# Kernel optimization log

Hardware: AMD Instinct MI355X
Metric: run time of the kernel (lower is better)

The kernel has to match this reference:

```python
import jax, jax.numpy as jnp
import numpy as np
from jax import lax

B, C_IN, C, H, W = 4, 256, 128, 64, 64
UP = (128, 128)
EPS = 1e-8  # torch CosineSimilarity eps


def _conv(x, w, b, p):
    y = lax.conv_general_dilated(x, w, (1, 1), [(p, p), (p, p)],
                                 dimension_numbers=('NCHW', 'OIHW', 'NCHW'))
    return y + b[None, :, None, None]


def _stdconv(x, w, b, s, o, p=0):
    # StdConv.forward = bn(act(conv(x))); eval-mode BatchNorm folded to per-channel affine (s, o)
    y = jax.nn.relu(_conv(x, w, b, p))
    return y * s[None, :, None, None] + o[None, :, None, None]


def _forward(t1, t2, t1_w, t1_b, t2_w, t2_b,
             df_res_w, df_res_b, df_res_s, df_res_o,
             df_b0_w, df_b0_b, df_b0_s, df_b0_o,
             df_b1_w, df_b1_b, df_b1_s, df_b1_o,
             df_fu_w, df_fu_b, df_fu_s, df_fu_o,
             br1_w, br1_b, br2_w, br2_b,
             fu_w, fu_b, fu_s, fu_o):
    Bs, _, Hs, Ws = t1.shape
    res1 = _conv(t1, t1_w, t1_b, 0)                      # [B,C,H,W]
    res2 = _conv(t2, t2_w, t2_b, 0)
    # torch .contiguous().view(B,-1,c) on NCHW: plain row-major reshape (NOT a transpose)
    f1 = res1.reshape(Bs, Hs * Ws, C)
    f2 = res2.reshape(Bs, Hs * Ws, C)
    num = jnp.sum(f1 * f2, axis=-1)
    den = jnp.maximum(jnp.linalg.norm(f1, axis=-1) * jnp.linalg.norm(f2, axis=-1), EPS)
    sim = (num / den)[..., None]                          # [B,HW,1]
    dif_w = 1.0 - sim

    def to_img(f):  # permute(0,2,1).view(B,C,H,W)
        return jnp.transpose(f, (0, 2, 1)).reshape(Bs, C, Hs, Ws)

    sim1 = to_img(f1 * sim) + res1
    sim2 = to_img(f2 * sim) + res2
    dif1 = to_img(f1 * dif_w) + res1
    dif2 = to_img(f2 * dif_w) + res2
    # AvgPool2d(kernel=2, stride=2)
    simp = jnp.abs(sim1 - sim2).reshape(Bs, C, Hs // 2, 2, Ws // 2, 2).mean(axis=(3, 5))
    # InceptionConv(2C -> C, branch=2)
    x = jnp.concatenate([dif1, dif2], axis=1)
    r = _stdconv(x, df_res_w, df_res_b, df_res_s, df_res_o, 0)
    b0 = _stdconv(r, df_b0_w, df_b0_b, df_b0_s, df_b0_o, 1)   # 3x3
    b1 = _stdconv(r, df_b1_w, df_b1_b, df_b1_s, df_b1_o, 2)   # 5x5
    dif = _stdconv(jnp.concatenate([b0, b1], axis=1), df_fu_w, df_fu_b, df_fu_s, df_fu_o, 0) + r
    N = (Hs // 2) * (Ws // 2)
    attn = simp.reshape(Bs, N, C)                         # [B,N,C]

    def branch_attn(inc):
        br = inc.reshape(Bs, C, Hs * Ws)                  # [B,C,HW]
        a = jax.nn.softmax(jnp.einsum('bnc,bcm->bnm', attn, br), axis=-1)  # [B,N,HW]
        return jnp.einsum('bnc,bnm->bcm', attn, a).reshape(Bs, C, Hs, Ws) + inc

    inc1 = _conv(dif, br1_w, br1_b, 1)
    inc2 = _conv(dif, br2_w, br2_b, 2)
    a1 = branch_attn(inc1)
    a2 = branch_attn(inc2)
    fused = _stdconv(jnp.concatenate([a1, a2], axis=1), fu_w, fu_b, fu_s, fu_o, 0) + dif
    # F.interpolate(..., mode='bilinear', align_corners=False) == jax bilinear resize
    return jax.image.resize(fused, (Bs, C, UP[0], UP[1]), method='bilinear')


def setup_inputs():
    key = jax.random.key(0)
    ks = iter(jax.random.split(key, 40))
    rn = lambda shape, sc=0.05: jax.random.normal(next(ks), shape, jnp.float32) * sc
    return {
        't1': jax.random.normal(next(ks), (B, C_IN, H, W), jnp.float32),
        't2': jax.random.normal(next(ks), (B, C_IN, H, W), jnp.float32),
        't1_w': rn((C, C_IN, 1, 1)), 't1_b': rn((C,)),
        't2_w': rn((C, C_IN, 1, 1)), 't2_b': rn((C,)),
        'df_res_w': rn((C, 2 * C, 1, 1)), 'df_res_b': rn((C,)), 'df_res_s': 1.0 + rn((C,)), 'df_res_o': rn((C,)),
        'df_b0_w': rn((C // 2, C, 3, 3)), 'df_b0_b': rn((C // 2,)), 'df_b0_s': 1.0 + rn((C // 2,)), 'df_b0_o': rn((C // 2,)),
        'df_b1_w': rn((C // 2, C, 5, 5)), 'df_b1_b': rn((C // 2,)), 'df_b1_s': 1.0 + rn((C // 2,)), 'df_b1_o': rn((C // 2,)),
        'df_fu_w': rn((C, C, 1, 1)), 'df_fu_b': rn((C,)), 'df_fu_s': 1.0 + rn((C,)), 'df_fu_o': rn((C,)),
        'br1_w': rn((C, C, 3, 3)), 'br1_b': rn((C,)),
        'br2_w': rn((C, C, 5, 5)), 'br2_b': rn((C,)),
        'fu_w': rn((C, 2 * C, 1, 1)), 'fu_b': rn((C,)), 'fu_s': 1.0 + rn((C,)), 'fu_o': rn((C,)),
    }


def reference(t1, t2, t1_w, t1_b, t2_w, t2_b,
              df_res_w, df_res_b, df_res_s, df_res_o,
              df_b0_w, df_b0_b, df_b0_s, df_b0_o,
              df_b1_w, df_b1_b, df_b1_s, df_b1_o,
              df_fu_w, df_fu_b, df_fu_s, df_fu_o,
              br1_w, br1_b, br2_w, br2_b,
              fu_w, fu_b, fu_s, fu_o):
    return _forward(t1, t2, t1_w, t1_b, t2_w, t2_b,
                    df_res_w, df_res_b, df_res_s, df_res_o,
                    df_b0_w, df_b0_b, df_b0_s, df_b0_o,
                    df_b1_w, df_b1_b, df_b1_s, df_b1_o,
                    df_fu_w, df_fu_b, df_fu_s, df_fu_o,
                    br1_w, br1_b, br2_w, br2_b,
                    fu_w, fu_b, fu_s, fu_o)
```

## Files before the change

### kernel.cpp

```cpp
#include <hip/hip_runtime.h>
#include <math.h>

#define HW 4096

typedef __attribute__((ext_vector_type(8))) short short8;
typedef __attribute__((ext_vector_type(4))) float floatx4;
typedef __attribute__((ext_vector_type(2))) float floatx2;

__device__ inline unsigned short f2bf(float f) {
    unsigned int u = __float_as_uint(f);
    unsigned int r = (u + 0x7fffu + ((u >> 16) & 1u)) >> 16;
    return (unsigned short)r;
}
__device__ inline float bf2f(unsigned short u) {
    return __uint_as_float(((unsigned int)u) << 16);
}


__device__ inline void prepack_dev(const float* __restrict__ w, unsigned short* __restrict__ wp,
                                   int CO, int CI, int KK, int i)
{
    if (i >= CO * CI * KK) return;
    int ci = i % CI;
    int t = i / CI;
    int co = t % CO;
    int kk = t / CO;
    int ti = (kk * (CO >> 4) + (co >> 4)) * (CI >> 5) + (ci >> 5);
    wp[(size_t)ti * 512 + ((ci >> 3) & 3) * 128 + (co & 15) * 8 + (ci & 7)]
        = f2bf(w[(co * CI + ci) * KK + kk]);
}

__global__ void setup_kernel(uint4* __restrict__ zp, int zn,
                             const float* __restrict__ w0, unsigned short* __restrict__ wp0,
                             const float* __restrict__ w1, unsigned short* __restrict__ wp1,
                             const float* __restrict__ w2, unsigned short* __restrict__ wp2,
                             const float* __restrict__ w3, unsigned short* __restrict__ wp3)
{
    int bx = blockIdx.x, tid = threadIdx.x;
    if (bx < 2312) {
        int i = bx * 256 + tid;
        if (i < zn) zp[i] = make_uint4(0u, 0u, 0u, 0u);
    } else if (bx < 2600) {
        prepack_dev(w0, wp0, 64, 128, 9,  (bx - 2312) * 256 + tid);
    } else if (bx < 3400) {
        prepack_dev(w1, wp1, 64, 128, 25, (bx - 2600) * 256 + tid);
    } else if (bx < 3976) {
        prepack_dev(w2, wp2, 128, 128, 9, (bx - 3400) * 256 + tid);
    } else {
        prepack_dev(w3, wp3, 128, 128, 25,(bx - 3976) * 256 + tid);
    }
}

__global__ void __launch_bounds__(256)
conv1x1_v2(const float* __restrict__ in, const float* __restrict__ w,
           const float* __restrict__ bias, float* __restrict__ out,
           int CI, int CO, int do_affine,
           const float* __restrict__ s, const float* __restrict__ o,
           const float* __restrict__ addbuf, unsigned short* __restrict__ xt)
{
    __shared__ float wl[2048];
    int tid = threadIdx.x;
    int c0 = blockIdx.y * 8;
    int b = blockIdx.z;
    for (int i = tid; i < CI * 8; i += 256) {
        int k = i & 7, ci = i >> 3;
        wl[i] = w[(c0 + k) * CI + ci];
    }
    __syncthreads();
    int m = blockIdx.x * 512 + tid * 2;
    floatx2 acc[8];
#pragma unroll
    for (int k = 0; k < 8; ++k) {
        float bv = bias[c0 + k];
        acc[k] = (floatx2){bv, bv};
    }
    const float* inb = in + (size_t)b * CI * HW + m;
#pragma unroll 4
    for (int ci = 0; ci < CI; ++ci) {
        floatx2 v = *(const floatx2*)(inb + (size_t)ci * HW);
#pragma unroll
        for (int k = 0; k < 8; ++k) acc[k] += wl[ci * 8 + k] * v;
    }
#pragma unroll
    for (int k = 0; k < 8; ++k) {
        floatx2 v = acc[k];
        if (do_affine) {
            float sc = s[c0 + k], of = o[c0 + k];
            v[0] = fmaxf(v[0], 0.f) * sc + of;
            v[1] = fmaxf(v[1], 0.f) * sc + of;
        }
        size_t oidx = ((size_t)(b * CO + c0 + k)) * HW + m;
        if (addbuf) v += *(const floatx2*)(addbuf + oidx);
        *(floatx2*)(out + oidx) = v;
        acc[k] = v;
    }
    if (xt) {
#pragma unroll
        for (int r = 0; r < 2; ++r) {
            int mm = m + r;
            union { unsigned short u16[8]; uint4 q; } pk;
#pragma unroll
            for (int k = 0; k < 8; ++k) pk.u16[k] = f2bf(acc[k][r]);
            int h = mm >> 6, wc = mm & 63;
            *(uint4*)(xt + ((size_t)(b * 16 + (c0 >> 3)) * 4624 + (h + 2) * 68 + (wc + 2)) * 8) = pk.q;
        }
    }
}

template<int K, int CO, int NB, int MS>
__global__ void __launch_bounds__(256)
convk_mfma(const unsigned short* __restrict__ xt, const unsigned short* __restrict__ wp,
           const float* __restrict__ bias, float* __restrict__ out,
           int OB, int co_off, int do_affine,
           const float* __restrict__ s, const float* __restrict__ o,
           unsigned short* __restrict__ incT)
{
    constexpr int CI = 128;
    constexpr int PAD = K / 2;
    constexpr int RO = 2 - PAD;
    constexpr int MT = 4 / MS;
    constexpr int CO16 = CO >> 4;
    constexpr int CI32 = CI >> 5;
    int tid = threadIdx.x;
    int wave = tid >> 6, lane = tid & 63;
    int h = blockIdx.x / MS, msb = blockIdx.x % MS;
    int b = blockIdx.y;
    int co0 = wave * 16 * NB;
    int n = lane & 15, q = lane >> 4;
    floatx4 acc[MT][NB];
#pragma unroll
    for (int mt = 0; mt < MT; ++mt)
#pragma unroll
        for (int nt = 0; nt < NB; ++nt) acc[mt][nt] = (floatx4){0.f, 0.f, 0.f, 0.f};

    const unsigned short* xb = xt + (size_t)(b * 16) * 4624 * 8;
    int mbase = msb * MT * 16;
    for (int ci0 = 0; ci0 < CI; ci0 += 32) {
#pragma unroll
        for (int kh = 0; kh < K; ++kh) {
            const unsigned short* xrow = xb + (size_t)(((ci0 >> 3) + q) * 4624 + (h + kh + RO) * 68 + RO) * 8;
            const unsigned short* wkh = wp + ((size_t)(kh * K) * CO16 * CI32 + (ci0 >> 5)) * 512 + lane * 8;
#pragma unroll
            for (int kw = 0; kw < K; ++kw) {
                short8 bfr[NB];
#pragma unroll
                for (int nt = 0; nt < NB; ++nt)
                    bfr[nt] = *(const short8*)(wkh + (size_t)((kw * CO16 + (co0 >> 4) + nt) * CI32) * 512);
#pragma unroll
                for (int mt = 0; mt < MT; ++mt) {
                    short8 afr = *(const short8*)(xrow + (mbase + mt * 16 + n + kw) * 8);
#pragma unroll
                    for (int nt = 0; nt < NB; ++nt)
                        acc[mt][nt] = __builtin_amdgcn_mfma_f32_16x16x32_bf16(afr, bfr[nt], acc[mt][nt], 0, 0, 0);
                }
            }
        }
    }
    int px0 = h * 64 + mbase + q * 4;
#pragma unroll
    for (int nt = 0; nt < NB; ++nt) {
        int co = co0 + nt * 16 + n;
        float bi = bias[co];
        float sc = do_affine ? s[co] : 1.f;
        float of = do_affine ? o[co] : 0.f;
        float* ob = out + ((size_t)(b * OB + co_off + co)) * HW;
        unsigned short* tb = incT ? incT + (size_t)b * 524288 : nullptr;
        int cpart = (co >> 5) * 512 + ((co >> 3) & 3) * 128 + (co & 7);
#pragma unroll
        for (int mt = 0; mt < MT; ++mt)
#pragma unroll
            for (int r = 0; r < 4; ++r) {
                int px = px0 + mt * 16 + r;
                float v = acc[mt][nt][r] + bi;
                if (do_affine) v = fmaxf(v, 0.f) * sc + of;
                ob[px] = v;
                if (incT) tb[(size_t)((px >> 4) * 2048 + cpart + (px & 15) * 8)] = f2bf(v);
            }
    }
}

__global__ void sim_kernel(const float* __restrict__ r1, const float* __restrict__ r2,
                           float* __restrict__ sim)
{
    int gw = blockIdx.x * 4 + (threadIdx.x >> 6);
    int lane = threadIdx.x & 63;
    int b = gw >> 12, n = gw & 4095;
    const float* p1 = r1 + (size_t)b * 524288 + (size_t)n * 128;
    const float* p2 = r2 + (size_t)b * 524288 + (size_t)n * 128;
    float a0 = p1[lane], a1 = p1[lane + 64];
    float b0 = p2[lane], b1 = p2[lane + 64];
    float dot = a0 * b0 + a1 * b1;
    float n1 = a0 * a0 + a1 * a1;
    float n2 = b0 * b0 + b1 * b1;
    for (int m = 32; m; m >>= 1) {
        dot += __shfl_xor(dot, m);
        n1  += __shfl_xor(n1, m);
        n2  += __shfl_xor(n2, m);
    }
    if (lane == 0) sim[b * 4096 + n] = dot / fmaxf(sqrtf(n1) * sqrtf(n2), 1e-8f);
}

__global__ void __launch_bounds__(256)
x_kernel2(const float* __restrict__ r1, const float* __restrict__ r2,
          const float* __restrict__ sim, float* __restrict__ xo)
{
    __shared__ float ls1[32 * 129], ls2[32 * 129];
    int b = blockIdx.y, p0 = blockIdx.x * 32, tid = threadIdx.x;
    const float* F1 = r1 + (size_t)b * 524288;
    const float* F2 = r2 + (size_t)b * 524288;
    for (int i = tid; i < 32 * 128; i += 256) {
        int p = i >> 7, c = i & 127;
        ls1[p * 129 + c] = F1[p0 * 128 + i];
        ls2[p * 129 + c] = F2[p0 * 128 + i];
    }
    __syncthreads();
    for (int j = tid; j < 256 * 32; j += 256) {
        int p = j & 31, cc = j >> 5;
        int c = cc & 127;
        float sv = sim[b * 4096 + p0 + p];
        const float* F = (cc & 128) ? F2 : F1;
        float t1v = ((cc & 128) ? ls2 : ls1)[p * 129 + c];
        xo[(size_t)b * 1048576 + (size_t)cc * 4096 + p0 + p] = t1v * (1.f - sv) + F[(size_t)c * 4096 + p0 + p];
    }
}

__global__ void __launch_bounds__(256)
simp_kernel3(const float* __restrict__ r1, const float* __restrict__ r2,
             const float* __restrict__ sim, unsigned short* __restrict__ attn_pk)
{
    __shared__ float lsd[64 * 33];
    int b = blockIdx.y, h2 = blockIdx.x, cg = blockIdx.z, tid = threadIdx.x;
    const float* F1 = r1 + (size_t)b * 524288;
    const float* F2 = r2 + (size_t)b * 524288;
    const float* sb = sim + b * 4096;
    int w2 = tid & 31, cl = tid >> 5;
    float acc[4] = {};
    for (int dh = 0; dh < 2; ++dh) {
        int prow = h2 * 128 + dh * 64;
        __syncthreads();
        for (int i = tid; i < 64 * 32; i += 256) {
            int p = i >> 5, c = i & 31;
            size_t gi = (size_t)(prow + p) * 128 + cg * 32 + c;
            lsd[p * 33 + c] = F1[gi] - F2[gi];
        }
        __syncthreads();
#pragma unroll
        for (int k = 0; k < 4; ++k) {
            int c = cl + 8 * k;
            int cG = cg * 32 + c;
#pragma unroll
            for (int dw = 0; dw < 2; ++dw) {
                int pl = 2 * w2 + dw;
                int p = prow + pl;
                float d = lsd[pl * 33 + c] * sb[p]
                        + (F1[(size_t)cG * 4096 + p] - F2[(size_t)cG * 4096 + p]);
                acc[k] += fabsf(d);
            }
        }
    }
#pragma unroll
    for (int k = 0; k < 4; ++k) {
        int cG = cg * 32 + cl + 8 * k;
        int f = cG * 1024 + h2 * 32 + w2;
        int n = f >> 7, c = f & 127;
        attn_pk[(size_t)b * 131072 + ((n >> 4) * 4 + (c >> 5)) * 512
                + ((c >> 3) & 3) * 128 + (n & 15) * 8 + (c & 7)] = f2bf(acc[k] * 0.25f);
    }
}

__global__ void __launch_bounds__(256)
attnA_pass1(const unsigned short* __restrict__ attn_pk,
            const unsigned short* __restrict__ incT1, const unsigned short* __restrict__ incT2,
            float* __restrict__ pmax, float* __restrict__ psum)
{
    __shared__ float lm[4][32], ls[4][32];
    int pair = blockIdx.y;
    int b = pair & 3, br = pair >> 2;
    int z = blockIdx.z;
    int tid = threadIdx.x;
    int wave = tid >> 6, lane = tid & 63;
    int n0 = blockIdx.x * 32;
    int q = lane >> 4;
    int col = lane & 15;
    const unsigned short* apk = attn_pk + (size_t)b * 131072 + (size_t)blockIdx.x * 4096 + lane * 8;
    short8 afrA[4], afrB[4];
#pragma unroll
    for (int kc = 0; kc < 4; ++kc) {
        afrA[kc] = *(const short8*)(apk + kc * 512);
        afrB[kc] = *(const short8*)(apk + 2048 + kc * 512);
    }
    const unsigned short* ibp = (br ? incT2 : incT1) + (size_t)b * 524288 + lane * 8;
    short8 bbuf[2][4];
    {
        const unsigned short* brow = ibp + (size_t)(z * 64 + wave * 16) * 2048;
#pragma unroll
        for (int kc = 0; kc < 4; ++kc) bbuf[0][kc] = *(const short8*)(brow + kc * 512);
        brow += 2048;
#pragma unroll
        for (int kc = 0; kc < 4; ++kc) bbuf[1][kc] = *(const short8*)(brow + kc * 512);
    }
    float rmA[4], rsA[4], rmB[4], rsB[4];
#pragma unroll
    for (int r = 0; r < 4; ++r) { rmA[r] = -3.0e38f; rsA[r] = 0.f; rmB[r] = -3.0e38f; rsB[r] = 0.f; }
#pragma unroll
    for (int mt = 0; mt < 16; ++mt) {
        const int cur = mt & 1;
        floatx4 accA = (floatx4){0.f, 0.f, 0.f, 0.f};
        floatx4 accB = (floatx4){0.f, 0.f, 0.f, 0.f};
#pragma unroll
        for (int kc = 0; kc < 4; ++kc) {
            accA = __builtin_amdgcn_mfma_f32_16x16x32_bf16(afrA[kc], bbuf[cur][kc], accA, 0, 0, 0);
            accB = __builtin_amdgcn_mfma_f32_16x16x32_bf16(afrB[kc], bbuf[cur][kc], accB, 0, 0, 0);
        }
        if (mt < 14) {
            const unsigned short* brow = ibp + (size_t)(z * 64 + wave * 16 + mt + 2) * 2048;
#pragma unroll
            for (int kc = 0; kc < 4; ++kc) bbuf[cur][kc] = *(const short8*)(brow + kc * 512);
        }
#pragma unroll
        for (int r = 0; r < 4; ++r) {
            float vA = accA[r];
            float nmA = fmaxf(rmA[r], vA);
            rsA[r] = rsA[r] * __expf(rmA[r] - nmA) + __expf(vA - nmA);
            rmA[r] = nmA;
            float vB = accB[r];
            float nmB = fmaxf(rmB[r], vB);
            rsB[r] = rsB[r] * __expf(rmB[r] - nmB) + __expf(vB - nmB);
            rmB[r] = nmB;
        }
    }
#pragma unroll
    for (int d = 1; d < 16; d <<= 1) {
#pragma unroll
        for (int r = 0; r < 4; ++r) {
            float om = __shfl_xor(rmA[r], d);
            float os = __shfl_xor(rsA[r], d);
            float nm = fmaxf(rmA[r], om);
            rsA[r] = rsA[r] * __expf(rmA[r] - nm) + os * __expf(om - nm);
            rmA[r] = nm;
            om = __shfl_xor(rmB[r], d);
            os = __shfl_xor(rsB[r], d);
            nm = fmaxf(rmB[r], om);
            rsB[r] = rsB[r] * __expf(rmB[r] - nm) + os * __expf(om - nm);
            rmB[r] = nm;
        }
    }
    if (col == 0) {
#pragma unroll
        for (int r = 0; r < 4; ++r) {
            lm[wave][q * 4 + r] = rmA[r];      ls[wave][q * 4 + r] = rsA[r];
            lm[wave][16 + q * 4 + r] = rmB[r]; ls[wave][16 + q * 4 + r] = rsB[r];
        }
    }
    __syncthreads();
    if (tid < 32) {
        float bm = lm[0][tid], bs = ls[0][tid];
        for (int w = 1; w < 4; ++w) {
            float om = lm[w][tid], os = ls[w][tid];
            float nm = fmaxf(bm, om);
            bs = bs * __expf(bm - nm) + os * __expf(om - nm);
            bm = nm;
        }
        pmax[((size_t)pair * 4 + z) * 1024 + n0 + tid] = bm;
        psum[((size_t)pair * 4 + z) * 1024 + n0 + tid] = bs;
    }
}

__global__ void attnA_scale2(const unsigned short* __restrict__ attn_pk,
                             const float* __restrict__ pmax, const float* __restrict__ psum,
                             float* __restrict__ mx, unsigned short* __restrict__ attnS_pk)
{
    int i = blockIdx.x * 256 + threadIdx.x;
    int pair = i >> 17;
    int o = i & 131071;
    int j = o & 7, lane = (o >> 3) & 63, ct = (o >> 9) & 7, kcn = o >> 12;
    int c = ct * 16 + (lane & 15);
    int n = kcn * 32 + (lane >> 4) * 8 + j;
    int b = pair & 3;
    float bm = pmax[((size_t)pair * 4) * 1024 + n];
    float bs = psum[((size_t)pair * 4) * 1024 + n];
#pragma unroll
    for (int z = 1; z < 4; ++z) {
        float om = pmax[((size_t)pair * 4 + z) * 1024 + n];
        float os = psum[((size_t)pair * 4 + z) * 1024 + n];
        float nm = fmaxf(bm, om);
        bs = bs * __expf(bm - nm) + os * __expf(om - nm);
        bm = nm;
    }
    if (c == 0) mx[pair * 1024 + n] = bm;
    float rc = 1.f / bs;
    int ii = b * 131072 + ((n >> 4) * 4 + (c >> 5)) * 512
           + ((c >> 3) & 3) * 128 + (n & 15) * 8 + (c & 7);
    attnS_pk[(size_t)i] = f2bf(bf2f(attn_pk[ii]) * rc);
}

__global__ void __launch_bounds__(256)
attn_passB4(const unsigned short* __restrict__ attn_pk,
            const unsigned short* __restrict__ attnS_pk,
            const unsigned short* __restrict__ incT1, const unsigned short* __restrict__ incT2,
            const float* __restrict__ mx,
            const float* __restrict__ inc1, const float* __restrict__ inc2,
            float* __restrict__ abuf)
{
    __shared__ unsigned short lp[4][16 * 36];
    __shared__ float lred[2][2048];
    int pair = blockIdx.y;
    int b = pair & 3, br = pair >> 2;
    int tid = threadIdx.x;
    int wv = tid >> 6, lane = tid & 63;
    int q = lane >> 4, col = lane & 15;
    int msub = wv & 1, nh = wv >> 1;
    int m0 = blockIdx.x * 32 + msub * 16;
    int mtg = m0 >> 4;
    const unsigned short* ibp = (br ? incT2 : incT1) + (size_t)b * 524288 + lane * 8;
    short8 bfrS[4];
#pragma unroll
    for (int kc = 0; kc < 4; ++kc)
        bfrS[kc] = *(const short8*)(ibp + (size_t)(mtg * 4 + kc) * 512);
    const float* mxp = mx + pair * 1024 + nh * 512;
    const unsigned short* aspk = attnS_pk + (size_t)pair * 131072 + lane * 8;
    const unsigned short* apk = attn_pk + (size_t)b * 131072 + lane * 8;
    floatx4 oacc[8];
#pragma unroll
    for (int ct = 0; ct < 8; ++ct) oacc[ct] = (floatx4){0.f, 0.f, 0.f, 0.f};
    unsigned short* lw = lp[wv];

    short8 arP[2][2][4];
    short8 asP[2][8];
    floatx4 mxq[2][2];
    floatx4 sacc[2][2];

#pragma unroll
    for (int t = 0; t < 2; ++t)
#pragma unroll
        for (int kc = 0; kc < 4; ++kc)
            arP[0][t][kc] = *(const short8*)(apk + (size_t)(((nh * 32 + t) * 4 + kc)) * 512);
#pragma unroll
    for (int ct = 0; ct < 8; ++ct)
        asP[0][ct] = *(const short8*)(aspk + (size_t)((nh * 16) * 8 + ct) * 512);
#pragma unroll
    for (int t = 0; t < 2; ++t)
        mxq[0][t] = *(const floatx4*)(mxp + t * 16 + q * 4);
#pragma unroll
    for (int t = 0; t < 2; ++t) {
        floatx4 a = (floatx4){0.f, 0.f, 0.f, 0.f};
#pragma unroll
        for (int kc = 0; kc < 4; ++kc)
            a = __builtin_amdgcn_mfma_f32_16x16x32_bf16(arP[0][t][kc], bfrS[kc], a, 0, 0, 0);
        sacc[0][t] = a;
    }
#pragma unroll
    for (int t = 0; t < 2; ++t)
#pragma unroll
        for (int kc = 0; kc < 4; ++kc)
            arP[1][t][kc] = *(const short8*)(apk + (size_t)(((nh * 32 + 2 + t) * 4 + kc)) * 512);

#pragma unroll
    for (int nc = 0; nc < 16; ++nc) {
        const int cur = nc & 1, nxt = cur ^ 1;
#pragma unroll
        for (int t = 0; t < 2; ++t) {
            floatx4 sv = sacc[cur][t];
            floatx4 mv = mxq[cur][t];
            unsigned int p01 = (unsigned int)f2bf(__expf(sv[0] - mv[0]))
                             | ((unsigned int)f2bf(__expf(sv[1] - mv[1])) << 16);
            unsigned int p23 = (unsigned int)f2bf(__expf(sv[2] - mv[2]))
                             | ((unsigned int)f2bf(__expf(sv[3] - mv[3])) << 16);
            *(uint2*)&lw[col * 36 + t * 16 + q * 4] = make_uint2(p01, p23);
        }
        if (nc < 15) {
#pragma unroll
            for (int ct = 0; ct < 8; ++ct)
                asP[nxt][ct] = *(const short8*)(aspk + (size_t)(((nh * 16 + nc + 1) * 8 + ct)) * 512);
#pragma unroll
            for (int t = 0; t < 2; ++t)
                mxq[nxt][t] = *(const floatx4*)(mxp + (nc + 1) * 32 + t * 16 + q * 4);
        }
        short8 pb = *(const short8*)&lw[col * 36 + q * 8];
        if (nc < 15) {
#pragma unroll
            for (int t = 0; t < 2; ++t) {
                floatx4 a = (floatx4){0.f, 0.f, 0.f, 0.f};
#pragma unroll
                for (int kc = 0; kc < 4; ++kc)
                    a = __builtin_amdgcn_mfma_f32_16x16x32_bf16(arP[nxt][t][kc], bfrS[kc], a, 0, 0, 0);
                sacc[nxt][t] = a;
            }
        }
        if (nc < 14) {
#pragma unroll
            for (int t = 0; t < 2; ++t)
#pragma unroll
                for (int kc = 0; kc < 4; ++kc)
                    arP[cur][t][kc] = *(const short8*)(apk + (size_t)(((nh * 32 + (nc + 2) * 2 + t) * 4 + kc)) * 512);
        }
#pragma unroll
        for (int ct = 0; ct < 8; ++ct)
            oacc[ct] = __builtin_amdgcn_mfma_f32_16x16x32_bf16(asP[cur][ct], pb, oacc[ct], 0, 0, 0);
    }

    if (nh == 1) {
        float* lr = lred[msub];
#pragma unroll
        for (int ct = 0; ct < 8; ++ct)
#pragma unroll
            for (int r = 0; r < 4; ++r)
                lr[(ct * 16 + q * 4 + r) * 16 + col] = oacc[ct][r];
    }
    __syncthreads();
    if (nh == 0) {
        const float* lr = lred[msub];
        const float* resid = (br ? inc2 : inc1) + (size_t)b * 524288;
        float* op = abuf + ((size_t)(b * 256 + br * 128)) * 4096;
        int m = m0 + col;
#pragma unroll
        for (int ct = 0; ct < 8; ++ct)
#pragma unroll
            for (int r = 0; r < 4; ++r) {
                int row = ct * 16 + q * 4 + r;
                op[(size_t)row * 4096 + m] = oacc[ct][r] + lr[row * 16 + col]
                                           + resid[(size_t)row * 4096 + m];
            }
    }
}

__global__ void upsample_kernel(const float* __restrict__ in, float* __restrict__ out)
{
    int i = blockIdx.x * 256 + threadIdx.x;
    int x = i & 127, y = (i >> 7) & 127, bc = i >> 14;
    const float* ib = in + (size_t)bc * HW;
    float sy = 0.5f * y - 0.25f;
    float sx = 0.5f * x - 0.25f;
    int y0 = (int)floorf(sy); float ty = sy - y0;
    int x0 = (int)floorf(sx); float tx = sx - x0;
    int y0c = min(max(y0, 0), 63), y1c = min(max(y0 + 1, 0), 63);
    int x0c = min(max(x0, 0), 63), x1c = min(max(x0 + 1, 0), 63);
    float v00 = ib[y0c * 64 + x0c], v01 = ib[y0c * 64 + x1c];
    float v10 = ib[y1c * 64 + x0c], v11 = ib[y1c * 64 + x1c];
    out[i] = (1.f - ty) * ((1.f - tx) * v00 + tx * v01) + ty * ((1.f - tx) * v10 + tx * v11);
}

extern "C" void kernel_launch(void* const* d_in, const int* in_sizes, int n_in,
                              void* d_out, int out_size, void* d_ws, size_t ws_size,
                              hipStream_t stream)
{
    const float* t1       = (const float*)d_in[0];
    const float* t2       = (const float*)d_in[1];
    const float* t1_w     = (const float*)d_in[2];
    const float* t1_b     = (const float*)d_in[3];
    const float* t2_w     = (const float*)d_in[4];
    const float* t2_b     = (const float*)d_in[5];
    const float* df_res_w = (const float*)d_in[6];
    const float* df_res_b = (const float*)d_in[7];
    const float* df_res_s = (const float*)d_in[8];
    const float* df_res_o = (const float*)d_in[9];
    const float* df_b0_w  = (const float*)d_in[10];
    const float* df_b0_b  = (const float*)d_in[11];
    const float* df_b0_s  = (const float*)d_in[12];
    const float* df_b0_o  = (const float*)d_in[13];
    const float* df_b1_w  = (const float*)d_in[14];
    const float* df_b1_b  = (const float*)d_in[15];
    const float* df_b1_s  = (const float*)d_in[16];
    const float* df_b1_o  = (const float*)d_in[17];
    const float* df_fu_w  = (const float*)d_in[18];
    const float* df_fu_b  = (const float*)d_in[19];
    const float* df_fu_s  = (const float*)d_in[20];
    const float* df_fu_o  = (const float*)d_in[21];
    const float* br1_w    = (const float*)d_in[22];
    const float* br1_b    = (const float*)d_in[23];
    const float* br2_w    = (const float*)d_in[24];
    const float* br2_b    = (const float*)d_in[25];
    const float* fu_w     = (const float*)d_in[26];
    const float* fu_b     = (const float*)d_in[27];
    const float* fu_s     = (const float*)d_in[28];
    const float* fu_o     = (const float*)d_in[29];

    float* ws = (float*)d_ws;
    float* res1 = ws;
    float* res2 = ws + 2097152;
    float* xbuf = ws + 4194304;
    float* scr  = ws + 8388608;
    float* abuf = ws + 12582912;
    float* attnS_f = ws + 16777216;
    float* simv = ws + 17301504;
    float* mxb  = ws + 17317888;

    unsigned short* us     = (unsigned short*)scr;
    unsigned short* wp_b0  = us;
    unsigned short* wp_b1  = us + 73728;
    unsigned short* wp_br1 = us + 278528;
    unsigned short* wp_br2 = us + 425984;
    unsigned short* xt_r   = us + 851968;
    unsigned short* xt_dif = us + 3219456;
    unsigned short* incT1  = us + 5586944;
    unsigned short* incT2  = us + 851968;
    unsigned short* attn_bf= us + 7684096;
    float* scrF = scr;
    float* pmaxb = scrF + 4104192;
    float* psumb = scrF + 4136960;
    unsigned short* attnS  = (unsigned short*)attnS_f;

    dim3 blk(256);

    setup_kernel<<<5576, blk, 0, stream>>>((uint4*)xt_r, 591872,
                                           df_b0_w, wp_b0, df_b1_w, wp_b1,
                                           br1_w, wp_br1, br2_w, wp_br2);

    conv1x1_v2<<<dim3(8, 16, 4), blk, 0, stream>>>(t1, t1_w, t1_b, res1, 256, 128, 0, nullptr, nullptr, nullptr, nullptr);
    conv1x1_v2<<<dim3(8, 16, 4), blk, 0, stream>>>(t2, t2_w, t2_b, res2, 256, 128, 0, nullptr, nullptr, nullptr, nullptr);
    sim_kernel<<<4096, blk, 0, stream>>>(res1, res2, simv);
    x_kernel2<<<dim3(128, 4), blk, 0, stream>>>(res1, res2, simv, xbuf);
    simp_kernel3<<<dim3(32, 4, 4), blk, 0, stream>>>(res1, res2, simv, attn_bf);
    conv1x1_v2<<<dim3(8, 16, 4), blk, 0, stream>>>(xbuf, df_res_w, df_res_b, res1, 256, 128, 1, df_res_s, df_res_o, nullptr, xt_r);
    convk_mfma<3, 64, 1, 4><<<dim3(256, 4), blk, 0, stream>>>(xt_r, wp_b0, df_b0_b, res2, 128, 0, 1, df_b0_s, df_b0_o, nullptr);
    convk_mfma<5, 64, 1, 4><<<dim3(256, 4), blk, 0, stream>>>(xt_r, wp_b1, df_b1_b, res2, 128, 64, 1, df_b1_s, df_b1_o, nullptr);
    conv1x1_v2<<<dim3(8, 16, 4), blk, 0, stream>>>(res2, df_fu_w, df_fu_b, xbuf, 128, 128, 1, df_fu_s, df_fu_o, res1, xt_dif);
    convk_mfma<3, 128, 2, 4><<<dim3(256, 4), blk, 0, stream>>>(xt_dif, wp_br1, br1_b, res1, 128, 0, 0, nullptr, nullptr, incT1);
    convk_mfma<5, 128, 2, 4><<<dim3(256, 4), blk, 0, stream>>>(xt_dif, wp_br2, br2_b, res2, 128, 0, 0, nullptr, nullptr, incT2);
    attnA_pass1<<<dim3(32, 8, 4), blk, 0, stream>>>(attn_bf, incT1, incT2, pmaxb, psumb);
    attnA_scale2<<<4096, blk, 0, stream>>>(attn_bf, pmaxb, psumb, mxb, attnS);
    attn_passB4<<<dim3(128, 8), blk, 0, stream>>>(attn_bf, attnS, incT1, incT2, mxb, res1, res2, abuf);
    float* dif = xbuf;
    float* fused = xbuf + 2097152;
    conv1x1_v2<<<dim3(8, 16, 4), blk, 0, stream>>>(abuf, fu_w, fu_b, fused, 256, 128, 1, fu_s, fu_o, dif, nullptr);
    upsample_kernel<<<32768, blk, 0, stream>>>(fused, (float*)d_out);
}
```

Baseline: 537.7 us.

## Replace input 1x1 convs with bf16 MFMA GEMMs over prepacked activations

The two input 1x1 convolutions (256->128 channels) move from the fp32 scalar conv1x1_v2 kernel to a bf16 MFMA GEMM. New packX kernels convert t1/t2 to bf16 in an MFMA-friendly tiled layout, and the weights are prepacked inside the setup kernel. This trades extra pack passes over the inputs and bf16 rounding of activations for much cheaper matrix math.

```diff
diff --git a/kernel.cpp b/kernel.cpp
--- a/kernel.cpp
+++ b/kernel.cpp
@@ -34,7 +34,9 @@
                              const float* __restrict__ w0, unsigned short* __restrict__ wp0,
                              const float* __restrict__ w1, unsigned short* __restrict__ wp1,
                              const float* __restrict__ w2, unsigned short* __restrict__ wp2,
-                             const float* __restrict__ w3, unsigned short* __restrict__ wp3)
+                             const float* __restrict__ w3, unsigned short* __restrict__ wp3,
+                             const float* __restrict__ w4, unsigned short* __restrict__ wp4,
+                             const float* __restrict__ w5, unsigned short* __restrict__ wp5)
 {
     int bx = blockIdx.x, tid = threadIdx.x;
     if (bx < 2312) {
@@ -46,8 +48,55 @@
         prepack_dev(w1, wp1, 64, 128, 25, (bx - 2600) * 256 + tid);
     } else if (bx < 3976) {
         prepack_dev(w2, wp2, 128, 128, 9, (bx - 3400) * 256 + tid);
+    } else if (bx < 5576) {
+        prepack_dev(w3, wp3, 128, 128, 25,(bx - 3976) * 256 + tid);
+    } else if (bx < 5704) {
+        prepack_dev(w4, wp4, 128, 256, 1, (bx - 5576) * 256 + tid);
     } else {
-        prepack_dev(w3, wp3, 128, 128, 25,(bx - 3976) * 256 + tid);
+        prepack_dev(w5, wp5, 128, 256, 1, (bx - 5704) * 256 + tid);
+    }
+}
+
+__global__ void packX(const float* __restrict__ in, unsigned short* __restrict__ out)
+{
+    int i = blockIdx.x * 256 + threadIdx.x;
+    int b = i >> 20;
+    int j = i & 1048575;
+    int ci = j >> 12, px = j & 4095;
+    out[(size_t)b * 1048576 + ((size_t)((px >> 4) * 8 + (ci >> 5))) * 512
+        + ((ci >> 3) & 3) * 128 + (px & 15) * 8 + (ci & 7)] = f2bf(in[i]);
+}
+
+__global__ void __launch_bounds__(256)
+gemm1x1_t(const unsigned short* __restrict__ Xpk, const unsigned short* __restrict__ Wpk,
+          const float* __restrict__ bias, float* __restrict__ out)
+{
+    int tid = threadIdx.x;
+    int wv = tid >> 6, lane = tid & 63;
+    int q = lane >> 4, n = lane & 15;
+    int pxb = blockIdx.x;
+    int b = blockIdx.y;
+    int co0 = wv * 32;
+    const unsigned short* apk = Xpk + (size_t)b * 1048576 + (size_t)pxb * 8 * 512 + lane * 8;
+    const unsigned short* wpk = Wpk + (size_t)(co0 >> 4) * 8 * 512 + lane * 8;
+    floatx4 acc0 = (floatx4){0.f, 0.f, 0.f, 0.f};
+    floatx4 acc1 = (floatx4){0.f, 0.f, 0.f, 0.f};
+#pragma unroll
+    for (int kc = 0; kc < 8; ++kc) {
+        short8 a  = *(const short8*)(apk + kc * 512);
+        short8 b0 = *(const short8*)(wpk + kc * 512);
+        short8 b1 = *(const short8*)(wpk + 8 * 512 + kc * 512);
+        acc0 = __builtin_amdgcn_mfma_f32_16x16x32_bf16(a, b0, acc0, 0, 0, 0);
+        acc1 = __builtin_amdgcn_mfma_f32_16x16x32_bf16(a, b1, acc1, 0, 0, 0);
+    }
+    int px0 = pxb * 16 + q * 4;
+#pragma unroll
+    for (int nt = 0; nt < 2; ++nt) {
+        int co = co0 + nt * 16 + n;
+        float bi = bias[co];
+        floatx4 v = nt ? acc1 : acc0;
+        v[0] += bi; v[1] += bi; v[2] += bi; v[3] += bi;
+        *(floatx4*)(out + ((size_t)(b * 128 + co)) * 4096 + px0) = v;
     }
 }
 
@@ -599,15 +648,22 @@
     float* pmaxb = scrF + 4104192;
     float* psumb = scrF + 4136960;
     unsigned short* attnS  = (unsigned short*)attnS_f;
+    unsigned short* wp_t1 = (unsigned short*)attnS_f;
+    unsigned short* wp_t2 = wp_t1 + 32768;
+    unsigned short* t1pk  = (unsigned short*)xbuf;
+    unsigned short* t2pk  = t1pk + 4194304;
 
     dim3 blk(256);
 
-    setup_kernel<<<5576, blk, 0, stream>>>((uint4*)xt_r, 591872,
+    setup_kernel<<<5832, blk, 0, stream>>>((uint4*)xt_r, 591872,
                                            df_b0_w, wp_b0, df_b1_w, wp_b1,
-                                           br1_w, wp_br1, br2_w, wp_br2);
-
-    conv1x1_v2<<<dim3(8, 16, 4), blk, 0, stream>>>(t1, t1_w, t1_b, res1, 256, 128, 0, nullptr, nullptr, nullptr, nullptr);
-    conv1x1_v2<<<dim3(8, 16, 4), blk, 0, stream>>>(t2, t2_w, t2_b, res2, 256, 128, 0, nullptr, nullptr, nullptr, nullptr);
+                                           br1_w, wp_br1, br2_w, wp_br2,
+                                           t1_w, wp_t1, t2_w, wp_t2);
+    packX<<<16384, blk, 0, stream>>>(t1, t1pk);
+    packX<<<16384, blk, 0, stream>>>(t2, t2pk);
+
+    gemm1x1_t<<<dim3(256, 4), blk, 0, stream>>>(t1pk, wp_t1, t1_b, res1);
+    gemm1x1_t<<<dim3(256, 4), blk, 0, stream>>>(t2pk, wp_t2, t2_b, res2);
     sim_kernel<<<4096, blk, 0, stream>>>(res1, res2, simv);
     x_kernel2<<<dim3(128, 4), blk, 0, stream>>>(res1, res2, simv, xbuf);
     simp_kernel3<<<dim3(32, 4, 4), blk, 0, stream>>>(res1, res2, simv, attn_bf);
```

Result: faster. 495.0 us (-7.9%).
